# Kernel tuning notes

Hardware: AMD Instinct MI355X
Metric: run time of the kernel (lower is better)

Reference implementation:

```python
import jax, jax.numpy as jnp
import numpy as np

D = 1024        # in_features == out_features (square weight required by the module's broadcast)
E = 64          # num_experts
R = 8           # lora rank
T = 16384       # tokens
ALPHA = 1.0
SCALING = ALPHA / R


def setup_inputs() -> dict:
    key = jax.random.key(0)
    k_x, k_l, k_w, k_a = jax.random.split(key, 4)
    x = jax.random.normal(k_x, (T, D), dtype=jnp.float32)
    labels = jax.random.randint(k_l, (T,), 0, E, dtype=jnp.int64)
    W = jax.random.normal(k_w, (D, D), dtype=jnp.float32) * 0.02   # original_weight, treated as [in, out]
    A = jax.random.normal(k_a, (E, D, R), dtype=jnp.float32)        # nn.init.normal_
    B = jnp.zeros((E, R, D), dtype=jnp.float32)                     # torch.zeros init; nonzero for a useful baseline:
    B = jax.random.normal(jax.random.fold_in(key, 7), (E, R, D), dtype=jnp.float32) * 0.02
    bias = jnp.zeros((D,), dtype=jnp.float32)
    return {"x": x, "labels": labels, "W": W, "A": A, "B": B, "bias": bias}


def reference(x, labels, W, A, B, bias):
    # Original math per token i: y_i = x_i @ (W + scaling * A[l_i] @ B[l_i]) + bias
    # (dropout in eval mode = identity). Computed efficiently as shared base GEMM
    # plus a per-token rank-R correction, avoiding per-token dense [D,D] weights.
    base = x @ W                                       # [T, D]
    A_g = A[labels]                                    # [T, D, R] gathered per token
    B_g = B[labels]                                    # [T, R, D]
    xa = jnp.einsum('ti,tir->tr', x, A_g)              # [T, R]
    lora = jnp.einsum('tr,tro->to', xa, B_g)           # [T, D]
    return base + SCALING * lora + bias
```

## Files before the change

### kernel.cpp

```cpp
#include <hip/hip_runtime.h>
#include <hip/hip_bf16.h>
#include <stdint.h>

#define T_TOK 16384
#define D_DIM 1024
#define E_EXP 64
#define R_RANK 8
#define SCALE 0.125f

typedef __attribute__((ext_vector_type(8))) __bf16 bf16x8;
typedef __attribute__((ext_vector_type(4))) float f32x4;

__device__ __forceinline__ uint16_t bf16_rne(float f) {
  union { float f; uint32_t u; } v; v.f = f;
  return (uint16_t)((v.u + 0x7fffu + ((v.u >> 16) & 1u)) >> 16);
}

__device__ __forceinline__ float bf16_to_f(uint16_t h) {
  union { uint32_t u; float f; } v; v.u = ((uint32_t)h) << 16;
  return v.f;
}

__device__ __forceinline__ void gld_lds16(const void* g, void* l) {
  __builtin_amdgcn_global_load_lds(
      (const __attribute__((address_space(1))) uint32_t*)g,
      (__attribute__((address_space(3))) uint32_t*)l, 16, 0, 0);
}

__global__ __launch_bounds__(256) void k_prep_w(const float* __restrict__ W,
                                                uint16_t* __restrict__ Wt) {
  __shared__ float tile[32][33];
  const int t = threadIdx.x;
  const int r0 = blockIdx.y * 32, c0 = blockIdx.x * 32;
  const int r = t >> 3, c = (t & 7) * 4;
  float4 v = *(const float4*)(W + (size_t)(r0 + r) * D_DIM + c0 + c);
  tile[r][c + 0] = v.x; tile[r][c + 1] = v.y;
  tile[r][c + 2] = v.z; tile[r][c + 3] = v.w;
  __syncthreads();
  const int n = t >> 3;
  const int kk = (t & 7) * 4;
  ushort4 o;
  o.x = bf16_rne(tile[kk + 0][n]);
  o.y = bf16_rne(tile[kk + 1][n]);
  o.z = bf16_rne(tile[kk + 2][n]);
  o.w = bf16_rne(tile[kk + 3][n]);
  *(ushort4*)(Wt + (size_t)(c0 + n) * D_DIM + r0 + kk) = o;
}

__global__ __launch_bounds__(256) void k_prep_b(const float* __restrict__ B,
                                                uint16_t* __restrict__ Bb) {
  const int idx = blockIdx.x * 256 + threadIdx.x;
  const int e = idx >> 10, n = idx & 1023;
  const float* src = B + (size_t)e * (R_RANK * D_DIM) + n;
  ushort4 o0, o1;
  o0.x = bf16_rne(src[0 * D_DIM]); o0.y = bf16_rne(src[1 * D_DIM]);
  o0.z = bf16_rne(src[2 * D_DIM]); o0.w = bf16_rne(src[3 * D_DIM]);
  o1.x = bf16_rne(src[4 * D_DIM]); o1.y = bf16_rne(src[5 * D_DIM]);
  o1.z = bf16_rne(src[6 * D_DIM]); o1.w = bf16_rne(src[7 * D_DIM]);
  *(ushort4*)(Bb + (size_t)idx * 8) = o0;
  *(ushort4*)(Bb + (size_t)idx * 8 + 4) = o1;
}

__global__ __launch_bounds__(256) void k_prep_a(const float* __restrict__ A,
                                                uint16_t* __restrict__ At) {
  const int idx = blockIdx.x * 256 + threadIdx.x;
  const int e = idx >> 10, d = idx & 1023;
  const float* src = A + (size_t)idx * R_RANK;
  float4 p0 = *(const float4*)(src);
  float4 p1 = *(const float4*)(src + 4);
  uint16_t* dst = At + (size_t)e * (R_RANK * D_DIM) + d;
  dst[0 * D_DIM] = bf16_rne(p0.x);
  dst[1 * D_DIM] = bf16_rne(p0.y);
  dst[2 * D_DIM] = bf16_rne(p0.z);
  dst[3 * D_DIM] = bf16_rne(p0.w);
  dst[4 * D_DIM] = bf16_rne(p1.x);
  dst[5 * D_DIM] = bf16_rne(p1.y);
  dst[6 * D_DIM] = bf16_rne(p1.z);
  dst[7 * D_DIM] = bf16_rne(p1.w);
}

__global__ __launch_bounds__(256) void k_prep_x(const float* __restrict__ x,
                                                const int* __restrict__ labels,
                                                const uint16_t* __restrict__ At,
                                                uint16_t* __restrict__ xb,
                                                float* __restrict__ xa) {
  const int wid = threadIdx.x >> 6, lane = threadIdx.x & 63;
  const int tok = blockIdx.x * 4 + wid;
  const int lbl = labels[tok];
  const float* xrow = x + (size_t)tok * D_DIM;
  const uint16_t* Ab = At + (size_t)lbl * (R_RANK * D_DIM);
  float acc[8] = {0, 0, 0, 0, 0, 0, 0, 0};
#pragma unroll
  for (int it = 0; it < 4; ++it) {
    const int d = it * 256 + lane * 4;
    float4 xv = *(const float4*)(xrow + d);
    ushort4 o;
    o.x = bf16_rne(xv.x); o.y = bf16_rne(xv.y);
    o.z = bf16_rne(xv.z); o.w = bf16_rne(xv.w);
    *(ushort4*)(xb + (size_t)tok * D_DIM + d) = o;
#pragma unroll
    for (int r = 0; r < 8; ++r) {
      ushort4 av = *(const ushort4*)(Ab + r * D_DIM + d);
      acc[r] += xv.x * bf16_to_f(av.x) + xv.y * bf16_to_f(av.y) +
                xv.z * bf16_to_f(av.z) + xv.w * bf16_to_f(av.w);
    }
  }
#pragma unroll
  for (int off = 32; off >= 1; off >>= 1) {
#pragma unroll
    for (int r = 0; r < 8; ++r) acc[r] += __shfl_xor(acc[r], off);
  }
  if (lane == 0) {
    float4 q0 = {acc[0], acc[1], acc[2], acc[3]};
    float4 q1 = {acc[4], acc[5], acc[6], acc[7]};
    *(float4*)(xa + (size_t)tok * 8) = q0;
    *(float4*)(xa + (size_t)tok * 8 + 4) = q1;
  }
}

__global__ __launch_bounds__(256) void k_gemm(const uint16_t* __restrict__ xb,
                                              const uint16_t* __restrict__ Wt,
                                              const uint16_t* __restrict__ Bb,
                                              const float* __restrict__ xa,
                                              const int* __restrict__ labels,
                                              const float* __restrict__ bias,
                                              float* __restrict__ out) {
  __shared__ __align__(16) uint16_t As[128 * 32];
  __shared__ __align__(16) uint16_t Bs[128 * 32];
  __shared__ __align__(16) float xas[128][8];
  __shared__ int lbls[128];

  const int t = threadIdx.x;
  const int wid = t >> 6, lane = t & 63;

  const int bid = blockIdx.x;
  const int sid = (bid & 7) * 128 + (bid >> 3);
  const int m0 = (sid >> 3) * 128;
  const int n0 = (sid & 7) * 128;

  if (t < 128) lbls[t] = labels[m0 + t];
  {
    const int r = t >> 1, c = (t & 1) * 4;
    *(float4*)&xas[r][c] = *(const float4*)(xa + (size_t)(m0 + r) * 8 + c);
  }
  __syncthreads();

  f32x4 acc[4][4] = {};
  const int wr = wid >> 1, wc = wid & 1;
  const int row_h = t >> 2;
  const int seg = (t & 3) * 8;

  const int fr = lane & 15, fq = lane >> 4;

  for (int kt = 0; kt < 32; ++kt) {
    const int k0 = kt * 32;
    uint16_t* ldsA = As + wid * 512;
    uint16_t* ldsB = Bs + wid * 512;
    gld_lds16(xb + (size_t)(m0 + row_h) * D_DIM + k0 + seg, ldsA);
    gld_lds16(xb + (size_t)(m0 + 64 + row_h) * D_DIM + k0 + seg, ldsA + 2048);
    gld_lds16(Wt + (size_t)(n0 + row_h) * D_DIM + k0 + seg, ldsB);
    gld_lds16(Wt + (size_t)(n0 + 64 + row_h) * D_DIM + k0 + seg, ldsB + 2048);
    __syncthreads();

    bf16x8 af[4], bfr[4];
#pragma unroll
    for (int i = 0; i < 4; ++i) {
      af[i]  = *(const bf16x8*)(As + (wr * 64 + i * 16 + fr) * 32 + fq * 8);
      bfr[i] = *(const bf16x8*)(Bs + (wc * 64 + i * 16 + fr) * 32 + fq * 8);
    }
#pragma unroll
    for (int i = 0; i < 4; ++i)
#pragma unroll
      for (int j = 0; j < 4; ++j)
        acc[i][j] = __builtin_amdgcn_mfma_f32_16x16x32_bf16(af[i], bfr[j], acc[i][j], 0, 0, 0);
    __syncthreads();
  }

  float bv[4];
#pragma unroll
  for (int j = 0; j < 4; ++j) bv[j] = bias[n0 + wc * 64 + j * 16 + fr];

#pragma unroll
  for (int i = 0; i < 4; ++i) {
#pragma unroll
    for (int jj = 0; jj < 4; ++jj) {
      const int ml = wr * 64 + i * 16 + fq * 4 + jj;
      const int tokrow = m0 + ml;
      const int lbl = lbls[ml];
      const float xv0 = xas[ml][0], xv1 = xas[ml][1], xv2 = xas[ml][2], xv3 = xas[ml][3];
      const float xv4 = xas[ml][4], xv5 = xas[ml][5], xv6 = xas[ml][6], xv7 = xas[ml][7];
#pragma unroll
      for (int j = 0; j < 4; ++j) {
        const int n = n0 + wc * 64 + j * 16 + fr;
        const bf16x8 bb = *(const bf16x8*)(Bb + ((size_t)lbl * D_DIM + n) * 8);
        float dot = xv0 * (float)bb[0] + xv1 * (float)bb[1] + xv2 * (float)bb[2] +
                    xv3 * (float)bb[3] + xv4 * (float)bb[4] + xv5 * (float)bb[5] +
                    xv6 * (float)bb[6] + xv7 * (float)bb[7];
        out[(size_t)tokrow * D_DIM + n] = acc[i][j][jj] + bv[j] + SCALE * dot;
      }
    }
  }
}

extern "C" void kernel_launch(void* const* d_in, const int* in_sizes, int n_in,
                              void* d_out, int out_size, void* d_ws, size_t ws_size,
                              hipStream_t stream) {
  (void)in_sizes; (void)n_in; (void)out_size; (void)ws_size;
  const float* x      = (const float*)d_in[0];
  const int*   labels = (const int*)d_in[1];
  const float* W      = (const float*)d_in[2];
  const float* A      = (const float*)d_in[3];
  const float* B      = (const float*)d_in[4];
  const float* bias   = (const float*)d_in[5];
  float* out = (float*)d_out;

  uint8_t* ws = (uint8_t*)d_ws;
  uint16_t* xb = (uint16_t*)ws;
  uint16_t* Wt = (uint16_t*)(ws + (size_t)33554432);
  uint16_t* Bb = (uint16_t*)(ws + (size_t)35651584);
  float*    xa = (float*)   (ws + (size_t)36700160);
  uint16_t* At = (uint16_t*)(ws + (size_t)37224448);

  k_prep_w<<<dim3(32, 32), 256, 0, stream>>>(W, Wt);
  k_prep_b<<<256, 256, 0, stream>>>(B, Bb);
  k_prep_a<<<256, 256, 0, stream>>>(A, At);
  k_prep_x<<<4096, 256, 0, stream>>>(x, labels, At, xb, xa);
  k_gemm<<<1024, 256, 0, stream>>>(xb, Wt, Bb, xa, labels, bias, out);
}
```

Baseline: 199.2 us.

## Rewrite GEMM as 256x256 double-buffered pipelined kernel with swizzled LDS

Replaces the 128x128 tile, single-buffer GEMM with a 256x256 tile, 512-thread kernel. It uses double-buffered LDS with a K-step of 64, XOR-swizzled LDS layout, and an interleaved schedule that issues loads for the next quarter-tile while MFMAs run on the current one, with setprio around the MFMA blocks. The goal is to hide global-load latency and raise data reuse per block. In exchange it uses about 140KB of LDS and only 256 blocks, which limits occupancy. The x-prep kernel is also widened to 8-element vector loads.

```diff
diff --git a/kernel.cpp b/kernel.cpp
--- a/kernel.cpp
+++ b/kernel.cpp
@@ -14,11 +14,6 @@
 __device__ __forceinline__ uint16_t bf16_rne(float f) {
   union { float f; uint32_t u; } v; v.f = f;
   return (uint16_t)((v.u + 0x7fffu + ((v.u >> 16) & 1u)) >> 16);
-}
-
-__device__ __forceinline__ float bf16_to_f(uint16_t h) {
-  union { uint32_t u; float f; } v; v.u = ((uint32_t)h) << 16;
-  return v.f;
 }
 
 __device__ __forceinline__ void gld_lds16(const void* g, void* l) {
@@ -91,18 +86,24 @@
   const uint16_t* Ab = At + (size_t)lbl * (R_RANK * D_DIM);
   float acc[8] = {0, 0, 0, 0, 0, 0, 0, 0};
 #pragma unroll
-  for (int it = 0; it < 4; ++it) {
-    const int d = it * 256 + lane * 4;
-    float4 xv = *(const float4*)(xrow + d);
-    ushort4 o;
-    o.x = bf16_rne(xv.x); o.y = bf16_rne(xv.y);
-    o.z = bf16_rne(xv.z); o.w = bf16_rne(xv.w);
-    *(ushort4*)(xb + (size_t)tok * D_DIM + d) = o;
+  for (int it = 0; it < 2; ++it) {
+    const int d = it * 512 + lane * 8;
+    float4 xv0 = *(const float4*)(xrow + d);
+    float4 xv1 = *(const float4*)(xrow + d + 4);
+    ushort4 o0, o1;
+    o0.x = bf16_rne(xv0.x); o0.y = bf16_rne(xv0.y);
+    o0.z = bf16_rne(xv0.z); o0.w = bf16_rne(xv0.w);
+    o1.x = bf16_rne(xv1.x); o1.y = bf16_rne(xv1.y);
+    o1.z = bf16_rne(xv1.z); o1.w = bf16_rne(xv1.w);
+    *(ushort4*)(xb + (size_t)tok * D_DIM + d) = o0;
+    *(ushort4*)(xb + (size_t)tok * D_DIM + d + 4) = o1;
 #pragma unroll
     for (int r = 0; r < 8; ++r) {
-      ushort4 av = *(const ushort4*)(Ab + r * D_DIM + d);
-      acc[r] += xv.x * bf16_to_f(av.x) + xv.y * bf16_to_f(av.y) +
-                xv.z * bf16_to_f(av.z) + xv.w * bf16_to_f(av.w);
+      bf16x8 av = *(const bf16x8*)(Ab + r * D_DIM + d);
+      acc[r] += xv0.x * (float)av[0] + xv0.y * (float)av[1] +
+                xv0.z * (float)av[2] + xv0.w * (float)av[3] +
+                xv1.x * (float)av[4] + xv1.y * (float)av[5] +
+                xv1.z * (float)av[6] + xv1.w * (float)av[7];
     }
   }
 #pragma unroll
@@ -118,85 +119,143 @@
   }
 }
 
-__global__ __launch_bounds__(256) void k_gemm(const uint16_t* __restrict__ xb,
-                                              const uint16_t* __restrict__ Wt,
-                                              const uint16_t* __restrict__ Bb,
-                                              const float* __restrict__ xa,
-                                              const int* __restrict__ labels,
-                                              const float* __restrict__ bias,
-                                              float* __restrict__ out) {
-  __shared__ __align__(16) uint16_t As[128 * 32];
-  __shared__ __align__(16) uint16_t Bs[128 * 32];
-  __shared__ __align__(16) float xas[128][8];
-  __shared__ int lbls[128];
-
+#define ABUF_OFF 0
+#define BBUF_OFF 65536
+#define XAS_OFF  131072
+#define LBL_OFF  139264
+#define SMEM_BYTES 140288
+
+#define READ_A(bufv, a)                                                        \
+  {                                                                            \
+    _Pragma("unroll") for (int rm = 0; rm < 4; ++rm)                           \
+    _Pragma("unroll") for (int kk = 0; kk < 2; ++kk)                           \
+      af[rm][kk] = *(const bf16x8*)(smem + ABUF_OFF + (bufv) * 32768 +         \
+                                    (a) * 16384 + (rm * 32 + wr * 16 + fr) * 128 + \
+                                    (((kk * 4 + fq) ^ sx) * 16));              \
+  }
+
+#define READ_B(bufv, b)                                                        \
+  {                                                                            \
+    _Pragma("unroll") for (int rn = 0; rn < 2; ++rn)                           \
+    _Pragma("unroll") for (int kk = 0; kk < 2; ++kk)                           \
+      bfv[rn][kk] = *(const bf16x8*)(smem + BBUF_OFF + (bufv) * 32768 +        \
+                                     (b) * 16384 + (rn * 64 + wc * 16 + fr) * 128 + \
+                                     (((kk * 4 + fq) ^ sx) * 16));             \
+  }
+
+#define MMA(a, b)                                                              \
+  {                                                                            \
+    __builtin_amdgcn_s_setprio(1);                                             \
+    _Pragma("unroll") for (int rm = 0; rm < 4; ++rm)                           \
+    _Pragma("unroll") for (int rn = 0; rn < 2; ++rn)                           \
+    _Pragma("unroll") for (int kk = 0; kk < 2; ++kk)                           \
+      acc[(a) * 4 + rm][(b) * 2 + rn] = __builtin_amdgcn_mfma_f32_16x16x32_bf16( \
+          af[rm][kk], bfv[rn][kk], acc[(a) * 4 + rm][(b) * 2 + rn], 0, 0, 0);  \
+    __builtin_amdgcn_s_setprio(0);                                             \
+  }
+
+#define BAR() __builtin_amdgcn_s_barrier()
+#define LGKM0() asm volatile("s_waitcnt lgkmcnt(0)" ::: "memory")
+
+__global__ __launch_bounds__(512, 2) void k_gemm(const uint16_t* __restrict__ xb,
+                                                 const uint16_t* __restrict__ Wt,
+                                                 const uint16_t* __restrict__ Bb,
+                                                 const float* __restrict__ xa,
+                                                 const int* __restrict__ labels,
+                                                 const float* __restrict__ bias,
+                                                 float* __restrict__ out) {
+  __shared__ __align__(16) uint8_t smem[SMEM_BYTES];
   const int t = threadIdx.x;
   const int wid = t >> 6, lane = t & 63;
+  const int wr = wid >> 2, wc = wid & 3;
+  const int fr = lane & 15, fq = lane >> 4;
+  const int sx = fr & 7;
 
   const int bid = blockIdx.x;
-  const int sid = (bid & 7) * 128 + (bid >> 3);
-  const int m0 = (sid >> 3) * 128;
-  const int n0 = (sid & 7) * 128;
-
-  if (t < 128) lbls[t] = labels[m0 + t];
+  const int sid = (bid & 7) * 32 + (bid >> 3);
+  const int m0 = (sid >> 2) * 256;
+  const int n0 = (sid & 2047 & 3) * 256;
+
+  int* lbls = (int*)(smem + LBL_OFF);
+  float* xas = (float*)(smem + XAS_OFF);
+  if (t < 256) lbls[t] = labels[m0 + t];
   {
     const int r = t >> 1, c = (t & 1) * 4;
-    *(float4*)&xas[r][c] = *(const float4*)(xa + (size_t)(m0 + r) * 8 + c);
+    *(float4*)(xas + r * 8 + c) = *(const float4*)(xa + (size_t)(m0 + r) * 8 + c);
   }
   __syncthreads();
 
-  f32x4 acc[4][4] = {};
-  const int wr = wid >> 1, wc = wid & 1;
-  const int row_h = t >> 2;
-  const int seg = (t & 3) * 8;
-
-  const int fr = lane & 15, fq = lane >> 4;
-
-  for (int kt = 0; kt < 32; ++kt) {
-    const int k0 = kt * 32;
-    uint16_t* ldsA = As + wid * 512;
-    uint16_t* ldsB = Bs + wid * 512;
-    gld_lds16(xb + (size_t)(m0 + row_h) * D_DIM + k0 + seg, ldsA);
-    gld_lds16(xb + (size_t)(m0 + 64 + row_h) * D_DIM + k0 + seg, ldsA + 2048);
-    gld_lds16(Wt + (size_t)(n0 + row_h) * D_DIM + k0 + seg, ldsB);
-    gld_lds16(Wt + (size_t)(n0 + 64 + row_h) * D_DIM + k0 + seg, ldsB + 2048);
-    __syncthreads();
-
-    bf16x8 af[4], bfr[4];
-#pragma unroll
-    for (int i = 0; i < 4; ++i) {
-      af[i]  = *(const bf16x8*)(As + (wr * 64 + i * 16 + fr) * 32 + fq * 8);
-      bfr[i] = *(const bf16x8*)(Bs + (wc * 64 + i * 16 + fr) * 32 + fq * 8);
-    }
-#pragma unroll
-    for (int i = 0; i < 4; ++i)
-#pragma unroll
-      for (int j = 0; j < 4; ++j)
-        acc[i][j] = __builtin_amdgcn_mfma_f32_16x16x32_bf16(af[i], bfr[j], acc[i][j], 0, 0, 0);
-    __syncthreads();
+  const int srow = wid * 8 + (lane >> 3);
+  const int sslot = ((lane & 7) ^ ((lane >> 3) & 7)) * 8;
+  auto stA = [&](int kt, int h) {
+    const int buf = kt & 1;
+    const uint16_t* g = xb + (size_t)(m0 + h * 128 + srow) * D_DIM + kt * 64 + sslot;
+    uint8_t* l = smem + ABUF_OFF + buf * 32768 + h * 16384 + wid * 1024;
+    gld_lds16(g, l);
+    gld_lds16(g + (size_t)64 * D_DIM, l + 8192);
+  };
+  auto stB = [&](int kt, int h) {
+    const int buf = kt & 1;
+    const uint16_t* g = Wt + (size_t)(n0 + h * 128 + srow) * D_DIM + kt * 64 + sslot;
+    uint8_t* l = smem + BBUF_OFF + buf * 32768 + h * 16384 + wid * 1024;
+    gld_lds16(g, l);
+    gld_lds16(g + (size_t)64 * D_DIM, l + 8192);
+  };
+
+  f32x4 acc[8][4] = {};
+  bf16x8 af[4][2], bfv[2][2];
+
+  stA(0, 0); stB(0, 1); stA(0, 1); stB(0, 0); stA(1, 0); stB(1, 1);
+
+  for (int kt = 0; kt < 16; ++kt) {
+    const int buf = kt & 1;
+    const int kn1 = (kt + 1) & 15, kn2 = (kt + 2) & 15;
+    asm volatile("s_waitcnt vmcnt(4)" ::: "memory");
+    BAR();
+    READ_A(buf, 0); READ_B(buf, 0);
+    stA(kn1, 1);
+    BAR(); LGKM0();
+    MMA(0, 0);
+    BAR();
+    READ_B(buf, 1);
+    stB(kn1, 0);
+    BAR(); LGKM0();
+    MMA(0, 1);
+    BAR();
+    READ_A(buf, 1);
+    stA(kn2, 0);
+    BAR(); LGKM0();
+    MMA(1, 1);
+    BAR();
+    READ_B(buf, 0);
+    stB(kn2, 1);
+    BAR(); LGKM0();
+    MMA(1, 0);
+    BAR();
   }
 
   float bv[4];
 #pragma unroll
-  for (int j = 0; j < 4; ++j) bv[j] = bias[n0 + wc * 64 + j * 16 + fr];
-
-#pragma unroll
-  for (int i = 0; i < 4; ++i) {
-#pragma unroll
-    for (int jj = 0; jj < 4; ++jj) {
-      const int ml = wr * 64 + i * 16 + fq * 4 + jj;
-      const int tokrow = m0 + ml;
+  for (int rn = 0; rn < 4; ++rn) bv[rn] = bias[n0 + rn * 64 + wc * 16 + fr];
+
+#pragma unroll
+  for (int rm = 0; rm < 8; ++rm) {
+#pragma unroll
+    for (int j = 0; j < 4; ++j) {
+      const int ml = rm * 32 + wr * 16 + fq * 4 + j;
+      const int grow = m0 + ml;
       const int lbl = lbls[ml];
-      const float xv0 = xas[ml][0], xv1 = xas[ml][1], xv2 = xas[ml][2], xv3 = xas[ml][3];
-      const float xv4 = xas[ml][4], xv5 = xas[ml][5], xv6 = xas[ml][6], xv7 = xas[ml][7];
-#pragma unroll
-      for (int j = 0; j < 4; ++j) {
-        const int n = n0 + wc * 64 + j * 16 + fr;
+      const float* xv = xas + ml * 8;
+      const float x0 = xv[0], x1 = xv[1], x2 = xv[2], x3 = xv[3];
+      const float x4 = xv[4], x5 = xv[5], x6 = xv[6], x7 = xv[7];
+#pragma unroll
+      for (int rn = 0; rn < 4; ++rn) {
+        const int n = n0 + rn * 64 + wc * 16 + fr;
         const bf16x8 bb = *(const bf16x8*)(Bb + ((size_t)lbl * D_DIM + n) * 8);
-        float dot = xv0 * (float)bb[0] + xv1 * (float)bb[1] + xv2 * (float)bb[2] +
-                    xv3 * (float)bb[3] + xv4 * (float)bb[4] + xv5 * (float)bb[5] +
-                    xv6 * (float)bb[6] + xv7 * (float)bb[7];
-        out[(size_t)tokrow * D_DIM + n] = acc[i][j][jj] + bv[j] + SCALE * dot;
+        float dot = x0 * (float)bb[0] + x1 * (float)bb[1] + x2 * (float)bb[2] +
+                    x3 * (float)bb[3] + x4 * (float)bb[4] + x5 * (float)bb[5] +
+                    x6 * (float)bb[6] + x7 * (float)bb[7];
+        out[(size_t)grow * D_DIM + n] = acc[rm][rn][j] + bv[rn] + SCALE * dot;
       }
     }
   }
@@ -225,5 +284,5 @@
   k_prep_b<<<256, 256, 0, stream>>>(B, Bb);
   k_prep_a<<<256, 256, 0, stream>>>(A, At);
   k_prep_x<<<4096, 256, 0, stream>>>(x, labels, At, xb, xa);
-  k_gemm<<<1024, 256, 0, stream>>>(xb, Wt, Bb, xa, labels, bias, out);
-}
+  k_gemm<<<256, 512, 0, stream>>>(xb, Wt, Bb, xa, labels, bias, out);
+}
```

Measured after the change: 177.2 us. -11.1%, faster.
